# Performance work log

Hardware: AMD Instinct MI355X
Metric: run time of the kernel (lower is better)

The kernel has to match this reference:

```python
import jax, jax.numpy as jnp
import numpy as np

B, TQ, TK, E, H, DH = 4, 1024, 1024, 1024, 16, 64
EPS = 1e-5

def setup_inputs() -> dict:
    key = jax.random.key(0)
    ks = jax.random.split(key, 16)
    s = 0.02
    return {
        "x": jax.random.normal(ks[0], (B, TQ, E), jnp.float32),
        "encoder_out": jax.random.normal(ks[1], (B, TK, E), jnp.float32),
        "Q1w": jax.random.normal(ks[2], (H, DH, E), jnp.float32) * s,
        "Q1b": jax.random.normal(ks[3], (H, DH), jnp.float32) * s,
        "Q2w": jax.random.normal(ks[4], (H, DH, E), jnp.float32) * s,
        "Q2b": jax.random.normal(ks[5], (H, DH), jnp.float32) * s,
        "K1w": jax.random.normal(ks[6], (H, DH, E), jnp.float32) * s,
        "K1b": jax.random.normal(ks[7], (H, DH), jnp.float32) * s,
        "K2w": jax.random.normal(ks[8], (H, DH, E), jnp.float32) * s,
        "K2b": jax.random.normal(ks[9], (H, DH), jnp.float32) * s,
        "Vw": jax.random.normal(ks[10], (H, DH, E), jnp.float32) * s,
        "Vb": jax.random.normal(ks[11], (H, DH), jnp.float32) * s,
        "lam": jax.random.uniform(ks[12], (H,), jnp.float32, 0.5, 1.0),
        "gn_gamma": jnp.ones((H * DH,), jnp.float32),
        "gn_beta": jnp.zeros((H * DH,), jnp.float32),
        "out_w": jax.random.normal(ks[13], (E, H * DH), jnp.float32) * s,
        "out_b": jax.random.normal(ks[14], (E,), jnp.float32) * s,
    }

def _proj(inp, w, b):
    # inp: [B,T,E], w: [H,DH,E] -> [B,H,T,DH]
    return jnp.einsum('bte,hde->bhtd', inp, w) + b[None, :, None, :]

def reference(x, encoder_out, Q1w, Q1b, Q2w, Q2b, K1w, K1b, K2w, K2b, Vw, Vb,
              lam, gn_gamma, gn_beta, out_w, out_b):
    scale = 1.0 / jnp.sqrt(jnp.float32(DH))
    q1 = _proj(x, Q1w, Q1b)
    q2 = _proj(x, Q2w, Q2b)
    k1 = _proj(encoder_out, K1w, K1b)
    k2 = _proj(encoder_out, K2w, K2b)
    v = _proj(encoder_out, Vw, Vb)
    s1 = jnp.einsum('bhtd,bhsd->bhts', q1, k1) * scale  # [B,H,TQ,TK]
    s2 = jnp.einsum('bhtd,bhsd->bhts', q2, k2) * scale
    w = jax.nn.softmax(s1, axis=-1) - lam[None, :, None, None] * jax.nn.softmax(s2, axis=-1)
    out = jnp.einsum('bhts,bhsd->bhtd', w, v)  # [B,H,TQ,DH]
    # GroupNorm(num_groups=H, channels=H*DH) over [B,C,T]: per (B,H) stats over (T,DH)
    mu = jnp.mean(out, axis=(2, 3), keepdims=True)
    var = jnp.mean(jnp.square(out - mu), axis=(2, 3), keepdims=True)
    normed = (out - mu) * jax.lax.rsqrt(var + EPS)
    g = gn_gamma.reshape(H, DH)[None, :, None, :]
    b_ = gn_beta.reshape(H, DH)[None, :, None, :]
    normed = normed * g + b_
    y = normed.transpose(0, 2, 1, 3).reshape(B, TQ, H * DH)
    return y @ out_w.T + out_b
```

## Files before the change

### kernel.cpp

```cpp
#include <hip/hip_runtime.h>
#include <cmath>

typedef __bf16 bf16_t;
typedef bf16_t bf16x8 __attribute__((ext_vector_type(8)));
typedef bf16_t bf16x4 __attribute__((ext_vector_type(4)));
typedef float  f32x4  __attribute__((ext_vector_type(4)));

#define Bn  4
#define TQn 1024
#define TKn 1024
#define En  1024
#define Hn  16
#define DHn 64

static constexpr float EPSv = 1e-5f;
static constexpr float C_SCALE = 0.18033688011112042f;

#define GLDS16(g, l)                                                         \
    __builtin_amdgcn_global_load_lds(                                        \
        (const __attribute__((address_space(1))) void*)(g),                  \
        (__attribute__((address_space(3))) void*)(l), 16, 0, 0)

__global__ __launch_bounds__(256)
void cvt_all(const float* __restrict__ x, const float* __restrict__ enc,
             const float* __restrict__ q1w, const float* __restrict__ q2w,
             const float* __restrict__ k1w, const float* __restrict__ k2w,
             const float* __restrict__ vw,  const float* __restrict__ outw,
             bf16_t* __restrict__ xb, bf16_t* __restrict__ encb,
             bf16_t* __restrict__ wq, bf16_t* __restrict__ wkv,
             bf16_t* __restrict__ wob)
{
    int idx = blockIdx.x * 256 + threadIdx.x;
    const float* src; bf16_t* dst;
    if      (idx < 1048576) { src = x    + (size_t)idx * 4;              dst = xb   + (size_t)idx * 4; }
    else if (idx < 2097152) { src = enc  + (size_t)(idx - 1048576) * 4;  dst = encb + (size_t)(idx - 1048576) * 4; }
    else if (idx < 2359296) { src = q1w  + (size_t)(idx - 2097152) * 4;  dst = wq   + (size_t)(idx - 2097152) * 4; }
    else if (idx < 2621440) { src = q2w  + (size_t)(idx - 2359296) * 4;  dst = wq   + 1048576 + (size_t)(idx - 2359296) * 4; }
    else if (idx < 2883584) { src = k1w  + (size_t)(idx - 2621440) * 4;  dst = wkv  + (size_t)(idx - 2621440) * 4; }
    else if (idx < 3145728) { src = k2w  + (size_t)(idx - 2883584) * 4;  dst = wkv  + 1048576 + (size_t)(idx - 2883584) * 4; }
    else if (idx < 3407872) { src = vw   + (size_t)(idx - 3145728) * 4;  dst = wkv  + 2097152 + (size_t)(idx - 3145728) * 4; }
    else                    { src = outw + (size_t)(idx - 3407872) * 4;  dst = wob  + (size_t)(idx - 3407872) * 4; }
    float4 v = *(const float4*)src;
    bf16x4 o;
    o[0] = (bf16_t)v.x; o[1] = (bf16_t)v.y; o[2] = (bf16_t)v.z; o[3] = (bf16_t)v.w;
    *(bf16x4*)dst = o;
}

__global__ __launch_bounds__(256, 3)
void gemm_proj(const bf16_t* __restrict__ xb, const bf16_t* __restrict__ encb,
               const bf16_t* __restrict__ wq, const bf16_t* __restrict__ wkv,
               const float* __restrict__ q1b, const float* __restrict__ q2b,
               const float* __restrict__ k1b, const float* __restrict__ k2b,
               const float* __restrict__ vb,
               bf16_t* __restrict__ q12, bf16_t* __restrict__ k12v)
{
    __shared__ bf16_t sA[128 * 64];
    __shared__ bf16_t sB[128 * 64];
    int bx = blockIdx.x;
    const bf16_t* A; const bf16_t* W; bf16_t* C; const float* bp; int blockN;
    if (bx < 16) {
        A = xb; W = wq; C = q12; blockN = bx << 7;
        bp = (blockN >> 10) ? q2b : q1b;
    } else {
        bx -= 16;
        A = encb; W = wkv; C = k12v; blockN = bx << 7;
        const int seg = blockN >> 10;
        bp = (seg == 0) ? k1b : ((seg == 1) ? k2b : vb);
    }
    const int blockM = blockIdx.y << 7;

    const int tid = threadIdx.x;
    const int w = tid >> 6, lane = tid & 63;
    const int q = lane >> 4, r = lane & 15;
    const int wm = w & 1, wn = w >> 1;

    f32x4 acc[4][4];
#pragma unroll
    for (int i = 0; i < 4; ++i)
#pragma unroll
        for (int j = 0; j < 4; ++j) acc[i][j] = (f32x4){0.f, 0.f, 0.f, 0.f};

    for (int k0 = 0; k0 < 1024; k0 += 64) {
#pragma unroll
        for (int c = 0; c < 4; ++c) {
            const int s = c * 256 + tid;
            const int row = s >> 3;
            const int cg = (s & 7) ^ (row & 7);
            GLDS16(A + (size_t)(blockM + row) * 1024 + k0 + cg * 8, sA + c * 2048 + w * 512);
            GLDS16(W + (size_t)(blockN + row) * 1024 + k0 + cg * 8, sB + c * 2048 + w * 512);
        }
        __syncthreads();
#pragma unroll
        for (int ks = 0; ks < 2; ++ks) {
            bf16x8 a[4], b[4];
#pragma unroll
            for (int i = 0; i < 4; ++i) {
                const int row = wm * 64 + i * 16 + r;
                const int g = (ks * 4 + q) ^ (row & 7);
                a[i] = *(const bf16x8*)&sA[row * 64 + g * 8];
            }
#pragma unroll
            for (int j = 0; j < 4; ++j) {
                const int row = wn * 64 + j * 16 + r;
                const int g = (ks * 4 + q) ^ (row & 7);
                b[j] = *(const bf16x8*)&sB[row * 64 + g * 8];
            }
#pragma unroll
            for (int i = 0; i < 4; ++i)
#pragma unroll
                for (int j = 0; j < 4; ++j)
                    acc[i][j] = __builtin_amdgcn_mfma_f32_16x16x32_bf16(a[i], b[j], acc[i][j], 0, 0, 0);
        }
        __syncthreads();
    }

    const int seg = blockN >> 10;
#pragma unroll
    for (int j = 0; j < 4; ++j) {
        const int n = blockN + wn * 64 + j * 16 + r;
        const float bv = bp[n & 1023];
#pragma unroll
        for (int i = 0; i < 4; ++i) {
            f32x4 v = acc[i][j];
#pragma unroll
            for (int e = 0; e < 4; ++e) {
                const int m = blockM + wm * 64 + i * 16 + q * 4 + e;
                const float val = v[e] + bv;
                const int bb = m >> 10, t = m & 1023;
                const int h = (n >> 6) & 15, d = n & 63;
                ((bf16_t*)C)[((((size_t)seg * 4 + bb) * 16 + h) * 1024 + t) * 64 + d] = (bf16_t)val;
            }
        }
    }
}

__global__ __launch_bounds__(256, 4)
void gemm_out(const bf16_t* __restrict__ yb, const bf16_t* __restrict__ wob,
              const float* __restrict__ outb, float* __restrict__ out)
{
    __shared__ bf16_t sA[64 * 64];
    __shared__ bf16_t sB[128 * 64];
    const int L = blockIdx.x;
    const int xcd = L & 7, kk = L >> 3;
    const int blockM = (xcd * 8 + (kk >> 3)) * 64;
    const int blockN = (kk & 7) * 128;

    const int tid = threadIdx.x;
    const int w = tid >> 6, lane = tid & 63;
    const int q = lane >> 4, r = lane & 15;

    f32x4 acc[4][2];
#pragma unroll
    for (int i = 0; i < 4; ++i)
#pragma unroll
        for (int j = 0; j < 2; ++j) acc[i][j] = (f32x4){0.f, 0.f, 0.f, 0.f};

    for (int k0 = 0; k0 < 1024; k0 += 64) {
#pragma unroll
        for (int c = 0; c < 2; ++c) {
            const int s = c * 256 + tid;
            const int row = s >> 3;
            const int cg = (s & 7) ^ (row & 7);
            GLDS16(yb + (size_t)(blockM + row) * 1024 + k0 + cg * 8, sA + c * 2048 + w * 512);
        }
#pragma unroll
        for (int c = 0; c < 4; ++c) {
            const int s = c * 256 + tid;
            const int row = s >> 3;
            const int cg = (s & 7) ^ (row & 7);
            GLDS16(wob + (size_t)(blockN + row) * 1024 + k0 + cg * 8, sB + c * 2048 + w * 512);
        }
        __syncthreads();
#pragma unroll
        for (int ks = 0; ks < 2; ++ks) {
            bf16x8 a[4], b[2];
#pragma unroll
            for (int i = 0; i < 4; ++i) {
                const int row = i * 16 + r;
                const int g = (ks * 4 + q) ^ (row & 7);
                a[i] = *(const bf16x8*)&sA[row * 64 + g * 8];
            }
#pragma unroll
            for (int j = 0; j < 2; ++j) {
                const int row = w * 32 + j * 16 + r;
                const int g = (ks * 4 + q) ^ (row & 7);
                b[j] = *(const bf16x8*)&sB[row * 64 + g * 8];
            }
#pragma unroll
            for (int i = 0; i < 4; ++i)
#pragma unroll
                for (int j = 0; j < 2; ++j)
                    acc[i][j] = __builtin_amdgcn_mfma_f32_16x16x32_bf16(a[i], b[j], acc[i][j], 0, 0, 0);
        }
        __syncthreads();
    }

#pragma unroll
    for (int j = 0; j < 2; ++j) {
        const int n = blockN + w * 32 + j * 16 + r;
        const float bv = outb[n];
#pragma unroll
        for (int i = 0; i < 4; ++i) {
            f32x4 v = acc[i][j];
#pragma unroll
            for (int e = 0; e < 4; ++e) {
                const int m = blockM + i * 16 + q * 4 + e;
                out[(size_t)m * 1024 + n] = v[e] + bv;
            }
        }
    }
}

__device__ __forceinline__ void compute_S(const bf16_t* __restrict__ sK,
                                          const bf16x8 (&fQ)[2],
                                          f32x4 (&S)[4], int q, int r)
{
#pragma unroll
    for (int i = 0; i < 4; ++i) S[i] = (f32x4){0.f, 0.f, 0.f, 0.f};
#pragma unroll
    for (int ks = 0; ks < 2; ++ks) {
        bf16x8 fK[4];
#pragma unroll
        for (int i = 0; i < 4; ++i) {
            const int row = i * 16 + r;
            const int g = (ks * 4 + q) ^ (row & 7);
            fK[i] = *(const bf16x8*)&sK[row * 64 + g * 8];
        }
        __builtin_amdgcn_s_setprio(1);
#pragma unroll
        for (int i = 0; i < 4; ++i)
            S[i] = __builtin_amdgcn_mfma_f32_16x16x32_bf16(fK[i], fQ[ks], S[i], 0, 0, 0);
        __builtin_amdgcn_s_setprio(0);
    }
}

__device__ __forceinline__ void softmax_pw(f32x4 (&S)[4], bf16_t* __restrict__ sPt,
                                           float& l, int w, int q, int r)
{
    const int t = w * 16 + r;
    float part = 0.f;
#pragma unroll
    for (int i = 0; i < 4; ++i) {
        bf16x4 pk;
#pragma unroll
        for (int e = 0; e < 4; ++e) {
            const float p = __builtin_amdgcn_exp2f(S[i][e] * C_SCALE);
            part += p;
            pk[e] = (bf16_t)p;
        }
        const int sb = i * 16 + q * 4;
        const int g = (sb >> 3) ^ (t & 7);
        *(bf16x4*)&sPt[t * 64 + g * 8 + (sb & 7)] = pk;
    }
    l += part;
}

__device__ __forceinline__ void pv(const bf16_t* __restrict__ sPt,
                                   const bf16x8 (&fV)[4][2],
                                   f32x4 (&O)[4], int w, int q, int r)
{
#pragma unroll
    for (int ks = 0; ks < 2; ++ks) {
        const int m = w * 16 + r;
        const int g = (ks * 4 + q) ^ (m & 7);
        bf16x8 fP = *(const bf16x8*)&sPt[m * 64 + g * 8];
        __builtin_amdgcn_s_setprio(1);
#pragma unroll
        for (int j = 0; j < 4; ++j)
            O[j] = __builtin_amdgcn_mfma_f32_16x16x32_bf16(fP, fV[j][ks], O[j], 0, 0, 0);
        __builtin_amdgcn_s_setprio(0);
    }
}

__global__ __launch_bounds__(512, 2)
void diff_attn_mfma(const bf16_t* __restrict__ q12, const bf16_t* __restrict__ k12v,
                    const float* __restrict__ lam, bf16_t* __restrict__ out,
                    float* __restrict__ stats)
{
    __shared__ bf16_t sK1[2][64 * 64];
    __shared__ bf16_t sK2[2][64 * 64];
    __shared__ bf16_t sVt[64 * 64];
    __shared__ bf16_t sPt[128 * 64];
    __shared__ float  sl1[128], sl2[128];
    __shared__ float  sred[16];

    const int tid = threadIdx.x;
    const int w = tid >> 6, lane = tid & 63;
    const int q = lane >> 4, r = lane & 15;
    const int bh = blockIdx.x, qt = blockIdx.y;
    const float lamv = lam[bh & (Hn - 1)];

    const size_t HT = (size_t)TKn * DHn;
    const bf16_t* q1g = q12 + (size_t)bh * HT + (size_t)qt * 128 * DHn;
    const bf16_t* q2g = q1g + 64 * HT;
    const bf16_t* k1g = k12v + (size_t)bh * HT;
    const bf16_t* k2g = k1g + 64 * HT;
    const bf16_t* vg  = k1g + 128 * HT;

    bf16x8 fQ1[2], fQ2[2];
    {
        const int t = w * 16 + r;
#pragma unroll
        for (int ks = 0; ks < 2; ++ks) {
            fQ1[ks] = *(const bf16x8*)(q1g + (size_t)t * 64 + ks * 32 + q * 8);
            fQ2[ks] = *(const bf16x8*)(q2g + (size_t)t * 64 + ks * 32 + q * 8);
        }
    }

    f32x4 O1[4], O2[4];
    float l1 = 0.f, l2 = 0.f;
#pragma unroll
    for (int j = 0; j < 4; ++j) { O1[j] = (f32x4){0.f,0.f,0.f,0.f}; O2[j] = (f32x4){0.f,0.f,0.f,0.f}; }

    {
        const int row = tid >> 3;
        const int cg = (tid & 7) ^ (row & 7);
        GLDS16(k1g + row * 64 + cg * 8, &sK1[0][tid * 8]);
        GLDS16(k2g + row * 64 + cg * 8, &sK2[0][tid * 8]);
        const int s = tid & 63;
        bf16x8 v0 = *(const bf16x8*)(vg + (size_t)s * 64 + w * 8);
#pragma unroll
        for (int i = 0; i < 8; ++i) {
            const int d = w * 8 + i;
            sVt[d * 64 + (((s >> 3) ^ i) << 3) + (s & 7)] = v0[i];
        }
        __syncthreads();
    }

    bf16x8 vr;
    for (int st = 0; st < TKn / 64; ++st) {
        const int cur = st & 1;
        if (st < 15) {
            const int row = tid >> 3;
            const int cg = (tid & 7) ^ (row & 7);
            GLDS16(k1g + (size_t)(st + 1) * 4096 + row * 64 + cg * 8, &sK1[cur ^ 1][tid * 8]);
            GLDS16(k2g + (size_t)(st + 1) * 4096 + row * 64 + cg * 8, &sK2[cur ^ 1][tid * 8]);
            vr = *(const bf16x8*)(vg + (size_t)(st + 1) * 4096 + (size_t)(tid & 63) * 64 + w * 8);
        }

        bf16x8 fV[4][2];
#pragma unroll
        for (int j = 0; j < 4; ++j)
#pragma unroll
            for (int ks = 0; ks < 2; ++ks) {
                const int d = j * 16 + r;
                const int g = (ks * 4 + q) ^ (d & 7);
                fV[j][ks] = *(const bf16x8*)&sVt[d * 64 + g * 8];
            }
        {
            f32x4 S[4];
            compute_S(sK1[cur], fQ1, S, q, r);
            softmax_pw(S, sPt, l1, w, q, r);
            pv(sPt, fV, O1, w, q, r);
        }
        {
            f32x4 S[4];
            compute_S(sK2[cur], fQ2, S, q, r);
            softmax_pw(S, sPt, l2, w, q, r);
            pv(sPt, fV, O2, w, q, r);
        }

        __syncthreads();
        if (st < 15) {
            const int s = tid & 63;
#pragma unroll
            for (int i = 0; i < 8; ++i) {
                const int d = w * 8 + i;
                sVt[d * 64 + (((s >> 3) ^ i) << 3) + (s & 7)] = vr[i];
            }
            __syncthreads();
        }
    }

    {
        float v1 = l1;
        v1 += __shfl_xor(v1, 16); v1 += __shfl_xor(v1, 32);
        float v2 = l2;
        v2 += __shfl_xor(v2, 16); v2 += __shfl_xor(v2, 32);
        if (q == 0) { sl1[w * 16 + r] = v1; sl2[w * 16 + r] = v2; }
    }

    bf16_t* op = out + ((size_t)bh * TQn + (size_t)qt * 128) * DHn;
    float ssum = 0.f, ssq = 0.f;
#pragma unroll
    for (int e = 0; e < 4; ++e) {
        const int t = w * 16 + q * 4 + e;
        const float inv1 = 1.0f / sl1[t];
        const float inv2 = lamv / sl2[t];
#pragma unroll
        for (int j = 0; j < 4; ++j) {
            const float o = O1[j][e] * inv1 - O2[j][e] * inv2;
            op[(size_t)t * 64 + j * 16 + r] = (bf16_t)o;
            ssum += o;
            ssq += o * o;
        }
    }
#pragma unroll
    for (int d = 1; d < 64; d <<= 1) {
        ssum += __shfl_xor(ssum, d);
        ssq  += __shfl_xor(ssq, d);
    }
    if (lane == 0) { sred[w] = ssum; sred[8 + w] = ssq; }
    __syncthreads();
    if (tid == 0) {
        float a = 0.f, b = 0.f;
#pragma unroll
        for (int k = 0; k < 8; ++k) { a += sred[k]; b += sred[8 + k]; }
        stats[(bh << 3) + qt]       = a;
        stats[512 + (bh << 3) + qt] = b;
    }
}

__global__ __launch_bounds__(256)
void gn_apply(const bf16_t* __restrict__ attn, const float* __restrict__ stats,
              const float* __restrict__ gamma, const float* __restrict__ beta,
              bf16_t* __restrict__ y)
{
    const int f = blockIdx.x * 256 + threadIdx.x;
    const int d8 = (f & 7) << 3;
    const int t  = (f >> 3) & 1023;
    const int bh = f >> 13;
    const int h  = bh & 15;
    const int b  = bh >> 4;
    const float* p1 = stats + (bh << 3);
    const float* p2 = stats + 512 + (bh << 3);
    float s1 = 0.f, s2 = 0.f;
#pragma unroll
    for (int k = 0; k < 8; ++k) { s1 += p1[k]; s2 += p2[k]; }
    const float mu = s1 * (1.f / 65536.f);
    const float var = s2 * (1.f / 65536.f) - mu * mu;
    const float rstd = rsqrtf(var + EPSv);
    bf16x8 v = *(const bf16x8*)&attn[((size_t)bh << 16) + t * 64 + d8];
    const int c = h * 64 + d8;
    const float* gp = gamma + c;
    const float* bp = beta + c;
    bf16x8 o;
#pragma unroll
    for (int i = 0; i < 8; ++i)
        o[i] = (bf16_t)(((float)v[i] - mu) * rstd * gp[i] + bp[i]);
    *(bf16x8*)&y[((size_t)(b * 1024 + t)) * 1024 + c] = o;
}

extern "C" void kernel_launch(void* const* d_in, const int* in_sizes, int n_in,
                              void* d_out, int out_size, void* d_ws, size_t ws_size,
                              hipStream_t stream)
{
    const float* x    = (const float*)d_in[0];
    const float* enc  = (const float*)d_in[1];
    const float* Q1w  = (const float*)d_in[2];
    const float* Q1b  = (const float*)d_in[3];
    const float* Q2w  = (const float*)d_in[4];
    const float* Q2b  = (const float*)d_in[5];
    const float* K1w  = (const float*)d_in[6];
    const float* K1b  = (const float*)d_in[7];
    const float* K2w  = (const float*)d_in[8];
    const float* K2b  = (const float*)d_in[9];
    const float* Vw   = (const float*)d_in[10];
    const float* Vb   = (const float*)d_in[11];
    const float* lam  = (const float*)d_in[12];
    const float* gng  = (const float*)d_in[13];
    const float* gnb  = (const float*)d_in[14];
    const float* outw = (const float*)d_in[15];
    const float* outb = (const float*)d_in[16];
    float* out = (float*)d_out;

    bf16_t* xb   = (bf16_t*)d_ws;
    bf16_t* encb = xb   + 4194304;
    bf16_t* wq   = encb + 4194304;
    bf16_t* wkv  = wq   + 2097152;
    bf16_t* wob  = wkv  + 3145728;
    bf16_t* q12  = wob  + 1048576;
    bf16_t* k12v = q12  + 8388608;
    bf16_t* attnb= xb;
    bf16_t* yb   = encb;
    float*  stats= (float*)wq;

    cvt_all<<<14336, 256, 0, stream>>>(x, enc, Q1w, Q2w, K1w, K2w, Vw, outw,
                                       xb, encb, wq, wkv, wob);

    gemm_proj<<<dim3(40, 32), 256, 0, stream>>>(xb, encb, wq, wkv,
                                                Q1b, Q2b, K1b, K2b, Vb, q12, k12v);

    diff_attn_mfma<<<dim3(64, 8), 512, 0, stream>>>(q12, k12v, lam, attnb, stats);

    gn_apply<<<2048, 256, 0, stream>>>(attnb, stats, gng, gnb, yb);

    gemm_out<<<512, 256, 0, stream>>>(yb, wob, outb, out);
}
```

Before: 251.2 us.

## Split differential attention into per-softmax stream kernels plus combine pass

The fused attention kernel, which computed both softmax branches in one 512-thread block, is split into a 256-thread kernel launched over a third grid dimension selecting branch 1 or 2. Each block now handles 32 query rows per wave. A new combine kernel subtracts the two partial outputs and computes the GroupNorm partial sums. The projection GEMM grid is also remapped to a 1D launch with an XCD-aware block swizzle, meant to improve L2 locality. The trade-off is an extra kernel launch, an extra bf16 round-trip of partial outputs through memory, and V being loaded and transposed twice, in exchange for more blocks and better occupancy.

```diff
diff --git a/kernel.cpp b/kernel.cpp
--- a/kernel.cpp
+++ b/kernel.cpp
@@ -56,7 +56,11 @@
 {
     __shared__ bf16_t sA[128 * 64];
     __shared__ bf16_t sB[128 * 64];
-    int bx = blockIdx.x;
+    const int L = blockIdx.x;
+    const int xcd = L & 7, o = L >> 3;
+    int bx = (xcd & 1) * 20 + (o % 20);
+    const int blockM = ((xcd >> 1) * 8 + (o / 20)) << 7;
+
     const bf16_t* A; const bf16_t* W; bf16_t* C; const float* bp; int blockN;
     if (bx < 16) {
         A = xb; W = wq; C = q12; blockN = bx << 7;
@@ -67,7 +71,6 @@
         const int seg = blockN >> 10;
         bp = (seg == 0) ? k1b : ((seg == 1) ? k2b : vb);
     }
-    const int blockM = blockIdx.y << 7;
 
     const int tid = threadIdx.x;
     const int w = tid >> 6, lane = tid & 63;
@@ -212,11 +215,13 @@
 }
 
 __device__ __forceinline__ void compute_S(const bf16_t* __restrict__ sK,
-                                          const bf16x8 (&fQ)[2],
-                                          f32x4 (&S)[4], int q, int r)
-{
-#pragma unroll
-    for (int i = 0; i < 4; ++i) S[i] = (f32x4){0.f, 0.f, 0.f, 0.f};
+                                          const bf16x8 (&fQ)[2][2],
+                                          f32x4 (&S)[4][2], int q, int r)
+{
+#pragma unroll
+    for (int i = 0; i < 4; ++i)
+#pragma unroll
+        for (int j = 0; j < 2; ++j) S[i][j] = (f32x4){0.f, 0.f, 0.f, 0.f};
 #pragma unroll
     for (int ks = 0; ks < 2; ++ks) {
         bf16x8 fK[4];
@@ -229,115 +234,144 @@
         __builtin_amdgcn_s_setprio(1);
 #pragma unroll
         for (int i = 0; i < 4; ++i)
-            S[i] = __builtin_amdgcn_mfma_f32_16x16x32_bf16(fK[i], fQ[ks], S[i], 0, 0, 0);
+#pragma unroll
+            for (int j = 0; j < 2; ++j)
+                S[i][j] = __builtin_amdgcn_mfma_f32_16x16x32_bf16(fK[i], fQ[j][ks], S[i][j], 0, 0, 0);
         __builtin_amdgcn_s_setprio(0);
     }
 }
 
-__device__ __forceinline__ void softmax_pw(f32x4 (&S)[4], bf16_t* __restrict__ sPt,
-                                           float& l, int w, int q, int r)
-{
-    const int t = w * 16 + r;
-    float part = 0.f;
-#pragma unroll
-    for (int i = 0; i < 4; ++i) {
-        bf16x4 pk;
-#pragma unroll
-        for (int e = 0; e < 4; ++e) {
-            const float p = __builtin_amdgcn_exp2f(S[i][e] * C_SCALE);
-            part += p;
-            pk[e] = (bf16_t)p;
-        }
-        const int sb = i * 16 + q * 4;
-        const int g = (sb >> 3) ^ (t & 7);
-        *(bf16x4*)&sPt[t * 64 + g * 8 + (sb & 7)] = pk;
-    }
-    l += part;
+__device__ __forceinline__ void softmax_pw(f32x4 (&S)[4][2], bf16_t* __restrict__ sPt,
+                                           float (&l)[2], int w, int q, int r)
+{
+#pragma unroll
+    for (int j = 0; j < 2; ++j) {
+        const int t = w * 32 + j * 16 + r;
+        float part = 0.f;
+#pragma unroll
+        for (int i = 0; i < 4; ++i) {
+            bf16x4 pk;
+#pragma unroll
+            for (int e = 0; e < 4; ++e) {
+                const float p = __builtin_amdgcn_exp2f(S[i][j][e] * C_SCALE);
+                part += p;
+                pk[e] = (bf16_t)p;
+            }
+            const int sb = i * 16 + q * 4;
+            const int g = (sb >> 3) ^ (t & 7);
+            *(bf16x4*)&sPt[t * 64 + g * 8 + (sb & 7)] = pk;
+        }
+        l[j] += part;
+    }
 }
 
 __device__ __forceinline__ void pv(const bf16_t* __restrict__ sPt,
                                    const bf16x8 (&fV)[4][2],
-                                   f32x4 (&O)[4], int w, int q, int r)
+                                   f32x4 (&O)[2][4], int w, int q, int r)
 {
 #pragma unroll
     for (int ks = 0; ks < 2; ++ks) {
-        const int m = w * 16 + r;
-        const int g = (ks * 4 + q) ^ (m & 7);
-        bf16x8 fP = *(const bf16x8*)&sPt[m * 64 + g * 8];
+        bf16x8 fP[2];
+#pragma unroll
+        for (int i2 = 0; i2 < 2; ++i2) {
+            const int m = w * 32 + i2 * 16 + r;
+            const int g = (ks * 4 + q) ^ (m & 7);
+            fP[i2] = *(const bf16x8*)&sPt[m * 64 + g * 8];
+        }
         __builtin_amdgcn_s_setprio(1);
 #pragma unroll
-        for (int j = 0; j < 4; ++j)
-            O[j] = __builtin_amdgcn_mfma_f32_16x16x32_bf16(fP, fV[j][ks], O[j], 0, 0, 0);
+        for (int i2 = 0; i2 < 2; ++i2)
+#pragma unroll
+            for (int j = 0; j < 4; ++j)
+                O[i2][j] = __builtin_amdgcn_mfma_f32_16x16x32_bf16(fP[i2], fV[j][ks], O[i2][j], 0, 0, 0);
         __builtin_amdgcn_s_setprio(0);
     }
 }
 
-__global__ __launch_bounds__(512, 2)
-void diff_attn_mfma(const bf16_t* __restrict__ q12, const bf16_t* __restrict__ k12v,
-                    const float* __restrict__ lam, bf16_t* __restrict__ out,
-                    float* __restrict__ stats)
-{
-    __shared__ bf16_t sK1[2][64 * 64];
-    __shared__ bf16_t sK2[2][64 * 64];
+__global__ __launch_bounds__(256, 3)
+void attn_stream(const bf16_t* __restrict__ q12, const bf16_t* __restrict__ k12v,
+                 const float* __restrict__ lam, bf16_t* __restrict__ opart)
+{
+    __shared__ bf16_t sK[2][64 * 64];
     __shared__ bf16_t sVt[64 * 64];
     __shared__ bf16_t sPt[128 * 64];
-    __shared__ float  sl1[128], sl2[128];
-    __shared__ float  sred[16];
+    __shared__ float  sl[128];
 
     const int tid = threadIdx.x;
     const int w = tid >> 6, lane = tid & 63;
     const int q = lane >> 4, r = lane & 15;
-    const int bh = blockIdx.x, qt = blockIdx.y;
-    const float lamv = lam[bh & (Hn - 1)];
+    const int bh = blockIdx.x, qt = blockIdx.y, mat = blockIdx.z;
+    const float fac = mat ? lam[bh & (Hn - 1)] : 1.0f;
 
     const size_t HT = (size_t)TKn * DHn;
-    const bf16_t* q1g = q12 + (size_t)bh * HT + (size_t)qt * 128 * DHn;
-    const bf16_t* q2g = q1g + 64 * HT;
-    const bf16_t* k1g = k12v + (size_t)bh * HT;
-    const bf16_t* k2g = k1g + 64 * HT;
-    const bf16_t* vg  = k1g + 128 * HT;
-
-    bf16x8 fQ1[2], fQ2[2];
+    const bf16_t* qg = q12 + (size_t)(mat * 64 + bh) * HT + (size_t)qt * 128 * DHn;
+    const bf16_t* kg = k12v + (size_t)(mat * 64 + bh) * HT;
+    const bf16_t* vg = k12v + (size_t)(128 + bh) * HT;
+
+    bf16x8 fQ[2][2];
+#pragma unroll
+    for (int j = 0; j < 2; ++j) {
+        const int t = w * 32 + j * 16 + r;
+#pragma unroll
+        for (int ks = 0; ks < 2; ++ks)
+            fQ[j][ks] = *(const bf16x8*)(qg + (size_t)t * 64 + ks * 32 + q * 8);
+    }
+
+    f32x4 O[2][4];
+    float l[2] = {0.f, 0.f};
+#pragma unroll
+    for (int i = 0; i < 2; ++i)
+#pragma unroll
+        for (int j = 0; j < 4; ++j) O[i][j] = (f32x4){0.f,0.f,0.f,0.f};
+
     {
-        const int t = w * 16 + r;
-#pragma unroll
-        for (int ks = 0; ks < 2; ++ks) {
-            fQ1[ks] = *(const bf16x8*)(q1g + (size_t)t * 64 + ks * 32 + q * 8);
-            fQ2[ks] = *(const bf16x8*)(q2g + (size_t)t * 64 + ks * 32 + q * 8);
-        }
-    }
-
-    f32x4 O1[4], O2[4];
-    float l1 = 0.f, l2 = 0.f;
-#pragma unroll
-    for (int j = 0; j < 4; ++j) { O1[j] = (f32x4){0.f,0.f,0.f,0.f}; O2[j] = (f32x4){0.f,0.f,0.f,0.f}; }
-
-    {
-        const int row = tid >> 3;
-        const int cg = (tid & 7) ^ (row & 7);
-        GLDS16(k1g + row * 64 + cg * 8, &sK1[0][tid * 8]);
-        GLDS16(k2g + row * 64 + cg * 8, &sK2[0][tid * 8]);
-        const int s = tid & 63;
-        bf16x8 v0 = *(const bf16x8*)(vg + (size_t)s * 64 + w * 8);
-#pragma unroll
-        for (int i = 0; i < 8; ++i) {
-            const int d = w * 8 + i;
-            sVt[d * 64 + (((s >> 3) ^ i) << 3) + (s & 7)] = v0[i];
-        }
-        __syncthreads();
-    }
-
-    bf16x8 vr;
+#pragma unroll
+        for (int c = 0; c < 2; ++c) {
+            const int s = c * 256 + tid;
+            const int row = s >> 3;
+            const int cg = (s & 7) ^ (row & 7);
+            GLDS16(kg + row * 64 + cg * 8, &sK[0][c * 2048 + w * 512]);
+        }
+        bf16x8 v0[2];
+#pragma unroll
+        for (int rep = 0; rep < 2; ++rep)
+            v0[rep] = *(const bf16x8*)(vg + (size_t)lane * 64 + (w * 2 + rep) * 8);
+        __syncthreads();
+#pragma unroll
+        for (int rep = 0; rep < 2; ++rep) {
+            const int d0 = (w * 2 + rep) * 8;
+#pragma unroll
+            for (int i = 0; i < 8; ++i) {
+                const int d = d0 + i;
+                sVt[d * 64 + (((lane >> 3) ^ i) << 3) + (lane & 7)] = v0[rep][i];
+            }
+        }
+        __syncthreads();
+    }
+
+    bf16x8 vr[2];
     for (int st = 0; st < TKn / 64; ++st) {
         const int cur = st & 1;
         if (st < 15) {
-            const int row = tid >> 3;
-            const int cg = (tid & 7) ^ (row & 7);
-            GLDS16(k1g + (size_t)(st + 1) * 4096 + row * 64 + cg * 8, &sK1[cur ^ 1][tid * 8]);
-            GLDS16(k2g + (size_t)(st + 1) * 4096 + row * 64 + cg * 8, &sK2[cur ^ 1][tid * 8]);
-            vr = *(const bf16x8*)(vg + (size_t)(st + 1) * 4096 + (size_t)(tid & 63) * 64 + w * 8);
-        }
-
+            const bf16_t* kp = kg + (size_t)(st + 1) * 4096;
+#pragma unroll
+            for (int c = 0; c < 2; ++c) {
+                const int s = c * 256 + tid;
+                const int row = s >> 3;
+                const int cg = (s & 7) ^ (row & 7);
+                GLDS16(kp + row * 64 + cg * 8, &sK[cur ^ 1][c * 2048 + w * 512]);
+            }
+            const bf16_t* vp = vg + (size_t)(st + 1) * 4096;
+#pragma unroll
+            for (int rep = 0; rep < 2; ++rep)
+                vr[rep] = *(const bf16x8*)(vp + (size_t)lane * 64 + (w * 2 + rep) * 8);
+        }
+
+        {
+            f32x4 S[4][2];
+            compute_S(sK[cur], fQ, S, q, r);
+            softmax_pw(S, sPt, l, w, q, r);
+        }
         bf16x8 fV[4][2];
 #pragma unroll
         for (int j = 0; j < 4; ++j)
@@ -347,67 +381,77 @@
                 const int g = (ks * 4 + q) ^ (d & 7);
                 fV[j][ks] = *(const bf16x8*)&sVt[d * 64 + g * 8];
             }
-        {
-            f32x4 S[4];
-            compute_S(sK1[cur], fQ1, S, q, r);
-            softmax_pw(S, sPt, l1, w, q, r);
-            pv(sPt, fV, O1, w, q, r);
-        }
-        {
-            f32x4 S[4];
-            compute_S(sK2[cur], fQ2, S, q, r);
-            softmax_pw(S, sPt, l2, w, q, r);
-            pv(sPt, fV, O2, w, q, r);
-        }
+        pv(sPt, fV, O, w, q, r);
 
         __syncthreads();
         if (st < 15) {
-            const int s = tid & 63;
-#pragma unroll
-            for (int i = 0; i < 8; ++i) {
-                const int d = w * 8 + i;
-                sVt[d * 64 + (((s >> 3) ^ i) << 3) + (s & 7)] = vr[i];
+#pragma unroll
+            for (int rep = 0; rep < 2; ++rep) {
+                const int d0 = (w * 2 + rep) * 8;
+#pragma unroll
+                for (int i = 0; i < 8; ++i) {
+                    const int d = d0 + i;
+                    sVt[d * 64 + (((lane >> 3) ^ i) << 3) + (lane & 7)] = vr[rep][i];
+                }
             }
             __syncthreads();
         }
     }
 
-    {
-        float v1 = l1;
+#pragma unroll
+    for (int j = 0; j < 2; ++j) {
+        float v1 = l[j];
         v1 += __shfl_xor(v1, 16); v1 += __shfl_xor(v1, 32);
-        float v2 = l2;
-        v2 += __shfl_xor(v2, 16); v2 += __shfl_xor(v2, 32);
-        if (q == 0) { sl1[w * 16 + r] = v1; sl2[w * 16 + r] = v2; }
-    }
-
-    bf16_t* op = out + ((size_t)bh * TQn + (size_t)qt * 128) * DHn;
+        if (q == 0) sl[w * 32 + j * 16 + r] = v1;
+    }
+    __syncthreads();
+
+    bf16_t* op = opart + (size_t)mat * 4194304 + ((size_t)bh * TQn + (size_t)qt * 128) * DHn;
+#pragma unroll
+    for (int i2 = 0; i2 < 2; ++i2)
+#pragma unroll
+        for (int e = 0; e < 4; ++e) {
+            const int t = w * 32 + i2 * 16 + q * 4 + e;
+            const float inv = fac / sl[t];
+#pragma unroll
+            for (int j = 0; j < 4; ++j)
+                op[(size_t)t * 64 + j * 16 + r] = (bf16_t)(O[i2][j][e] * inv);
+        }
+}
+
+__global__ __launch_bounds__(256)
+void combine(const bf16_t* __restrict__ opart, bf16_t* __restrict__ attnb,
+             float* __restrict__ stats)
+{
+    __shared__ float sred[8];
+    const int tid = threadIdx.x;
+    const int f = blockIdx.x * 256 + tid;
+    const size_t base = (size_t)f * 8;
+    bf16x8 a = *(const bf16x8*)&opart[base];
+    bf16x8 b = *(const bf16x8*)&opart[4194304 + base];
+    bf16x8 o;
     float ssum = 0.f, ssq = 0.f;
 #pragma unroll
-    for (int e = 0; e < 4; ++e) {
-        const int t = w * 16 + q * 4 + e;
-        const float inv1 = 1.0f / sl1[t];
-        const float inv2 = lamv / sl2[t];
-#pragma unroll
-        for (int j = 0; j < 4; ++j) {
-            const float o = O1[j][e] * inv1 - O2[j][e] * inv2;
-            op[(size_t)t * 64 + j * 16 + r] = (bf16_t)o;
-            ssum += o;
-            ssq += o * o;
-        }
-    }
+    for (int i = 0; i < 8; ++i) {
+        const float v = (float)a[i] - (float)b[i];
+        o[i] = (bf16_t)v;
+        ssum += v;
+        ssq += v * v;
+    }
+    *(bf16x8*)&attnb[base] = o;
 #pragma unroll
     for (int d = 1; d < 64; d <<= 1) {
         ssum += __shfl_xor(ssum, d);
         ssq  += __shfl_xor(ssq, d);
     }
-    if (lane == 0) { sred[w] = ssum; sred[8 + w] = ssq; }
+    const int w = tid >> 6;
+    if ((tid & 63) == 0) { sred[w] = ssum; sred[4 + w] = ssq; }
     __syncthreads();
     if (tid == 0) {
-        float a = 0.f, b = 0.f;
-#pragma unroll
-        for (int k = 0; k < 8; ++k) { a += sred[k]; b += sred[8 + k]; }
-        stats[(bh << 3) + qt]       = a;
-        stats[512 + (bh << 3) + qt] = b;
+        const int bh = blockIdx.x >> 5;
+        const int slot = blockIdx.x & 31;
+        stats[bh * 32 + slot]        = sred[0] + sred[1] + sred[2] + sred[3];
+        stats[2048 + bh * 32 + slot] = sred[4] + sred[5] + sred[6] + sred[7];
     }
 }
 
@@ -422,11 +466,16 @@
     const int bh = f >> 13;
     const int h  = bh & 15;
     const int b  = bh >> 4;
-    const float* p1 = stats + (bh << 3);
-    const float* p2 = stats + 512 + (bh << 3);
+    const float* p1 = stats + bh * 32;
+    const float* p2 = stats + 2048 + bh * 32;
     float s1 = 0.f, s2 = 0.f;
 #pragma unroll
-    for (int k = 0; k < 8; ++k) { s1 += p1[k]; s2 += p2[k]; }
+    for (int k = 0; k < 8; ++k) {
+        float4 u1 = *(const float4*)&p1[k * 4];
+        float4 u2 = *(const float4*)&p2[k * 4];
+        s1 += u1.x + u1.y + u1.z + u1.w;
+        s2 += u2.x + u2.y + u2.z + u2.w;
+    }
     const float mu = s1 * (1.f / 65536.f);
     const float var = s2 * (1.f / 65536.f) - mu * mu;
     const float rstd = rsqrtf(var + EPSv);
@@ -471,17 +520,20 @@
     bf16_t* wob  = wkv  + 3145728;
     bf16_t* q12  = wob  + 1048576;
     bf16_t* k12v = q12  + 8388608;
-    bf16_t* attnb= xb;
-    bf16_t* yb   = encb;
-    float*  stats= (float*)wq;
+    bf16_t* opart= xb;
+    bf16_t* attnb= wq;
+    float*  stats= (float*)(wq + 4194304);
+    bf16_t* yb   = xb;
 
     cvt_all<<<14336, 256, 0, stream>>>(x, enc, Q1w, Q2w, K1w, K2w, Vw, outw,
                                        xb, encb, wq, wkv, wob);
 
-    gemm_proj<<<dim3(40, 32), 256, 0, stream>>>(xb, encb, wq, wkv,
-                                                Q1b, Q2b, K1b, K2b, Vb, q12, k12v);
-
-    diff_attn_mfma<<<dim3(64, 8), 512, 0, stream>>>(q12, k12v, lam, attnb, stats);
+    gemm_proj<<<1280, 256, 0, stream>>>(xb, encb, wq, wkv,
+                                        Q1b, Q2b, K1b, K2b, Vb, q12, k12v);
+
+    attn_stream<<<dim3(64, 8, 2), 256, 0, stream>>>(q12, k12v, lam, opart);
+
+    combine<<<2048, 256, 0, stream>>>(opart, attnb, stats);
 
     gn_apply<<<2048, 256, 0, stream>>>(attnb, stats, gng, gnb, yb);
 
```

Result: slower. 265.4 us (+5.6%).

## Split attention block into two warp groups, one per softmax stream

Applied to the files above, without the earlier changes.

The attention kernel is reorganized so that warps 0-3 process the first softmax stream (Q1/K1) and warps 4-7 the second (Q2/K2), each warp now covering 32 query rows instead of 16, with separate P buffers. The second group passes its lambda-scaled output through shared memory to the first group, which combines the two, writes the result and computes the GroupNorm partial stats. This halves the serial per-warp chain of S/softmax/PV work and reuses each K/V fragment across two row tiles. The cost is more registers per warp, a larger shared-memory P buffer, and an fp32 exchange through LDS, while launch bounds ask for four blocks per CU.

```diff
diff --git a/kernel.cpp b/kernel.cpp
--- a/kernel.cpp
+++ b/kernel.cpp
@@ -57,6 +57,7 @@
     __shared__ bf16_t sA[128 * 64];
     __shared__ bf16_t sB[128 * 64];
     int bx = blockIdx.x;
+    const int blockM = blockIdx.y << 7;
     const bf16_t* A; const bf16_t* W; bf16_t* C; const float* bp; int blockN;
     if (bx < 16) {
         A = xb; W = wq; C = q12; blockN = bx << 7;
@@ -67,7 +68,6 @@
         const int seg = blockN >> 10;
         bp = (seg == 0) ? k1b : ((seg == 1) ? k2b : vb);
     }
-    const int blockM = blockIdx.y << 7;
 
     const int tid = threadIdx.x;
     const int w = tid >> 6, lane = tid & 63;
@@ -212,11 +212,13 @@
 }
 
 __device__ __forceinline__ void compute_S(const bf16_t* __restrict__ sK,
-                                          const bf16x8 (&fQ)[2],
-                                          f32x4 (&S)[4], int q, int r)
-{
-#pragma unroll
-    for (int i = 0; i < 4; ++i) S[i] = (f32x4){0.f, 0.f, 0.f, 0.f};
+                                          const bf16x8 (&fQ)[2][2],
+                                          f32x4 (&S)[4][2], int q, int r)
+{
+#pragma unroll
+    for (int i = 0; i < 4; ++i)
+#pragma unroll
+        for (int j = 0; j < 2; ++j) S[i][j] = (f32x4){0.f, 0.f, 0.f, 0.f};
 #pragma unroll
     for (int ks = 0; ks < 2; ++ks) {
         bf16x8 fK[4];
@@ -229,88 +231,106 @@
         __builtin_amdgcn_s_setprio(1);
 #pragma unroll
         for (int i = 0; i < 4; ++i)
-            S[i] = __builtin_amdgcn_mfma_f32_16x16x32_bf16(fK[i], fQ[ks], S[i], 0, 0, 0);
+#pragma unroll
+            for (int j = 0; j < 2; ++j)
+                S[i][j] = __builtin_amdgcn_mfma_f32_16x16x32_bf16(fK[i], fQ[j][ks], S[i][j], 0, 0, 0);
         __builtin_amdgcn_s_setprio(0);
     }
 }
 
-__device__ __forceinline__ void softmax_pw(f32x4 (&S)[4], bf16_t* __restrict__ sPt,
-                                           float& l, int w, int q, int r)
-{
-    const int t = w * 16 + r;
-    float part = 0.f;
-#pragma unroll
-    for (int i = 0; i < 4; ++i) {
-        bf16x4 pk;
-#pragma unroll
-        for (int e = 0; e < 4; ++e) {
-            const float p = __builtin_amdgcn_exp2f(S[i][e] * C_SCALE);
-            part += p;
-            pk[e] = (bf16_t)p;
-        }
-        const int sb = i * 16 + q * 4;
-        const int g = (sb >> 3) ^ (t & 7);
-        *(bf16x4*)&sPt[t * 64 + g * 8 + (sb & 7)] = pk;
-    }
-    l += part;
+__device__ __forceinline__ void softmax_pw(f32x4 (&S)[4][2], bf16_t* __restrict__ sPt,
+                                           float (&l)[2], int wv, int q, int r)
+{
+#pragma unroll
+    for (int j = 0; j < 2; ++j) {
+        const int t = wv * 32 + j * 16 + r;
+        float part = 0.f;
+#pragma unroll
+        for (int i = 0; i < 4; ++i) {
+            bf16x4 pk;
+#pragma unroll
+            for (int e = 0; e < 4; ++e) {
+                const float p = __builtin_amdgcn_exp2f(S[i][j][e] * C_SCALE);
+                part += p;
+                pk[e] = (bf16_t)p;
+            }
+            const int sb = i * 16 + q * 4;
+            const int g = (sb >> 3) ^ (t & 7);
+            *(bf16x4*)&sPt[t * 64 + g * 8 + (sb & 7)] = pk;
+        }
+        l[j] += part;
+    }
 }
 
 __device__ __forceinline__ void pv(const bf16_t* __restrict__ sPt,
                                    const bf16x8 (&fV)[4][2],
-                                   f32x4 (&O)[4], int w, int q, int r)
+                                   f32x4 (&O)[2][4], int wv, int q, int r)
 {
 #pragma unroll
     for (int ks = 0; ks < 2; ++ks) {
-        const int m = w * 16 + r;
-        const int g = (ks * 4 + q) ^ (m & 7);
-        bf16x8 fP = *(const bf16x8*)&sPt[m * 64 + g * 8];
+        bf16x8 fP[2];
+#pragma unroll
+        for (int i2 = 0; i2 < 2; ++i2) {
+            const int m = wv * 32 + i2 * 16 + r;
+            const int g = (ks * 4 + q) ^ (m & 7);
+            fP[i2] = *(const bf16x8*)&sPt[m * 64 + g * 8];
+        }
         __builtin_amdgcn_s_setprio(1);
 #pragma unroll
-        for (int j = 0; j < 4; ++j)
-            O[j] = __builtin_amdgcn_mfma_f32_16x16x32_bf16(fP, fV[j][ks], O[j], 0, 0, 0);
+        for (int i2 = 0; i2 < 2; ++i2)
+#pragma unroll
+            for (int j = 0; j < 4; ++j)
+                O[i2][j] = __builtin_amdgcn_mfma_f32_16x16x32_bf16(fP[i2], fV[j][ks], O[i2][j], 0, 0, 0);
         __builtin_amdgcn_s_setprio(0);
     }
 }
 
-__global__ __launch_bounds__(512, 2)
-void diff_attn_mfma(const bf16_t* __restrict__ q12, const bf16_t* __restrict__ k12v,
-                    const float* __restrict__ lam, bf16_t* __restrict__ out,
-                    float* __restrict__ stats)
+__global__ __launch_bounds__(512, 4)
+void diff_attn_fused8(const bf16_t* __restrict__ q12, const bf16_t* __restrict__ k12v,
+                      const float* __restrict__ lam, bf16_t* __restrict__ out,
+                      float* __restrict__ stats)
 {
     __shared__ bf16_t sK1[2][64 * 64];
     __shared__ bf16_t sK2[2][64 * 64];
     __shared__ bf16_t sVt[64 * 64];
-    __shared__ bf16_t sPt[128 * 64];
-    __shared__ float  sl1[128], sl2[128];
+    __shared__ bf16_t sPt[2][128 * 64];
+    __shared__ float  sl[2][128];
     __shared__ float  sred[16];
 
     const int tid = threadIdx.x;
     const int w = tid >> 6, lane = tid & 63;
+    const int st_id = w >> 2;
+    const int wv = w & 3;
     const int q = lane >> 4, r = lane & 15;
     const int bh = blockIdx.x, qt = blockIdx.y;
     const float lamv = lam[bh & (Hn - 1)];
 
     const size_t HT = (size_t)TKn * DHn;
-    const bf16_t* q1g = q12 + (size_t)bh * HT + (size_t)qt * 128 * DHn;
-    const bf16_t* q2g = q1g + 64 * HT;
+    const bf16_t* qg = q12 + (size_t)(st_id * 64 + bh) * HT + (size_t)qt * 128 * DHn;
+    const bf16_t* kg = k12v + (size_t)(st_id * 64 + bh) * HT;
     const bf16_t* k1g = k12v + (size_t)bh * HT;
     const bf16_t* k2g = k1g + 64 * HT;
     const bf16_t* vg  = k1g + 128 * HT;
-
-    bf16x8 fQ1[2], fQ2[2];
-    {
-        const int t = w * 16 + r;
-#pragma unroll
-        for (int ks = 0; ks < 2; ++ks) {
-            fQ1[ks] = *(const bf16x8*)(q1g + (size_t)t * 64 + ks * 32 + q * 8);
-            fQ2[ks] = *(const bf16x8*)(q2g + (size_t)t * 64 + ks * 32 + q * 8);
-        }
-    }
-
-    f32x4 O1[4], O2[4];
-    float l1 = 0.f, l2 = 0.f;
-#pragma unroll
-    for (int j = 0; j < 4; ++j) { O1[j] = (f32x4){0.f,0.f,0.f,0.f}; O2[j] = (f32x4){0.f,0.f,0.f,0.f}; }
+    (void)kg;
+
+    bf16x8 fQ[2][2];
+#pragma unroll
+    for (int j = 0; j < 2; ++j) {
+        const int t = wv * 32 + j * 16 + r;
+#pragma unroll
+        for (int ks = 0; ks < 2; ++ks)
+            fQ[j][ks] = *(const bf16x8*)(qg + (size_t)t * 64 + ks * 32 + q * 8);
+    }
+
+    f32x4 O[2][4];
+    float l[2] = {0.f, 0.f};
+#pragma unroll
+    for (int i = 0; i < 2; ++i)
+#pragma unroll
+        for (int j = 0; j < 4; ++j) O[i][j] = (f32x4){0.f,0.f,0.f,0.f};
+
+    const bf16_t* sKs = st_id ? &sK2[0][0] : &sK1[0][0];
+    bf16_t* sPs = &sPt[st_id][0];
 
     {
         const int row = tid >> 3;
@@ -319,6 +339,7 @@
         GLDS16(k2g + row * 64 + cg * 8, &sK2[0][tid * 8]);
         const int s = tid & 63;
         bf16x8 v0 = *(const bf16x8*)(vg + (size_t)s * 64 + w * 8);
+        __syncthreads();
 #pragma unroll
         for (int i = 0; i < 8; ++i) {
             const int d = w * 8 + i;
@@ -338,6 +359,11 @@
             vr = *(const bf16x8*)(vg + (size_t)(st + 1) * 4096 + (size_t)(tid & 63) * 64 + w * 8);
         }
 
+        {
+            f32x4 S[4][2];
+            compute_S(sKs + cur * 4096, fQ, S, q, r);
+            softmax_pw(S, sPs, l, wv, q, r);
+        }
         bf16x8 fV[4][2];
 #pragma unroll
         for (int j = 0; j < 4; ++j)
@@ -347,18 +373,7 @@
                 const int g = (ks * 4 + q) ^ (d & 7);
                 fV[j][ks] = *(const bf16x8*)&sVt[d * 64 + g * 8];
             }
-        {
-            f32x4 S[4];
-            compute_S(sK1[cur], fQ1, S, q, r);
-            softmax_pw(S, sPt, l1, w, q, r);
-            pv(sPt, fV, O1, w, q, r);
-        }
-        {
-            f32x4 S[4];
-            compute_S(sK2[cur], fQ2, S, q, r);
-            softmax_pw(S, sPt, l2, w, q, r);
-            pv(sPt, fV, O2, w, q, r);
-        }
+        pv(sPs, fV, O, wv, q, r);
 
         __syncthreads();
         if (st < 15) {
@@ -372,42 +387,58 @@
         }
     }
 
-    {
-        float v1 = l1;
+#pragma unroll
+    for (int j = 0; j < 2; ++j) {
+        float v1 = l[j];
         v1 += __shfl_xor(v1, 16); v1 += __shfl_xor(v1, 32);
-        float v2 = l2;
-        v2 += __shfl_xor(v2, 16); v2 += __shfl_xor(v2, 32);
-        if (q == 0) { sl1[w * 16 + r] = v1; sl2[w * 16 + r] = v2; }
-    }
-
-    bf16_t* op = out + ((size_t)bh * TQn + (size_t)qt * 128) * DHn;
+        if (q == 0) sl[st_id][wv * 32 + j * 16 + r] = v1;
+    }
+    __syncthreads();
+
+    float* xchg = (float*)&sPt[0][0];
+
+    if (st_id == 1) {
+#pragma unroll
+        for (int i2 = 0; i2 < 2; ++i2)
+#pragma unroll
+            for (int e = 0; e < 4; ++e) {
+                const int t = wv * 32 + i2 * 16 + q * 4 + e;
+                const float inv2 = lamv / sl[1][t];
+#pragma unroll
+                for (int j = 0; j < 4; ++j)
+                    xchg[t * 64 + j * 16 + r] = O[i2][j][e] * inv2;
+            }
+    }
+    __syncthreads();
+
     float ssum = 0.f, ssq = 0.f;
-#pragma unroll
-    for (int e = 0; e < 4; ++e) {
-        const int t = w * 16 + q * 4 + e;
-        const float inv1 = 1.0f / sl1[t];
-        const float inv2 = lamv / sl2[t];
-#pragma unroll
-        for (int j = 0; j < 4; ++j) {
-            const float o = O1[j][e] * inv1 - O2[j][e] * inv2;
-            op[(size_t)t * 64 + j * 16 + r] = (bf16_t)o;
-            ssum += o;
-            ssq += o * o;
-        }
-    }
-#pragma unroll
-    for (int d = 1; d < 64; d <<= 1) {
-        ssum += __shfl_xor(ssum, d);
-        ssq  += __shfl_xor(ssq, d);
-    }
-    if (lane == 0) { sred[w] = ssum; sred[8 + w] = ssq; }
+    if (st_id == 0) {
+        bf16_t* op = out + ((size_t)bh * TQn + (size_t)qt * 128) * DHn;
+#pragma unroll
+        for (int i2 = 0; i2 < 2; ++i2)
+#pragma unroll
+            for (int e = 0; e < 4; ++e) {
+                const int t = wv * 32 + i2 * 16 + q * 4 + e;
+                const float inv1 = 1.0f / sl[0][t];
+#pragma unroll
+                for (int j = 0; j < 4; ++j) {
+                    const float o = O[i2][j][e] * inv1 - xchg[t * 64 + j * 16 + r];
+                    op[(size_t)t * 64 + j * 16 + r] = (bf16_t)o;
+                    ssum += o;
+                    ssq += o * o;
+                }
+            }
+#pragma unroll
+        for (int d = 1; d < 64; d <<= 1) {
+            ssum += __shfl_xor(ssum, d);
+            ssq  += __shfl_xor(ssq, d);
+        }
+        if (lane == 0) { sred[wv] = ssum; sred[8 + wv] = ssq; }
+    }
     __syncthreads();
     if (tid == 0) {
-        float a = 0.f, b = 0.f;
-#pragma unroll
-        for (int k = 0; k < 8; ++k) { a += sred[k]; b += sred[8 + k]; }
-        stats[(bh << 3) + qt]       = a;
-        stats[512 + (bh << 3) + qt] = b;
+        stats[(bh << 3) + qt]       = sred[0] + sred[1] + sred[2] + sred[3];
+        stats[512 + (bh << 3) + qt] = sred[8] + sred[9] + sred[10] + sred[11];
     }
 }
 
@@ -481,7 +512,7 @@
     gemm_proj<<<dim3(40, 32), 256, 0, stream>>>(xb, encb, wq, wkv,
                                                 Q1b, Q2b, K1b, K2b, Vb, q12, k12v);
 
-    diff_attn_mfma<<<dim3(64, 8), 512, 0, stream>>>(q12, k12v, lam, attnb, stats);
+    diff_attn_fused8<<<dim3(64, 8), 512, 0, stream>>>(q12, k12v, lam, attnb, stats);
 
     gn_apply<<<2048, 256, 0, stream>>>(attnb, stats, gng, gnb, yb);
 
```

Measured after the change: 249.5 us. About the same (-0.7%).
